# Optimization experiments

Hardware: AMD Instinct MI355X
Metric: run time of the kernel (lower is better)

The kernel has to match this reference:

```python
import jax, jax.numpy as jnp
import numpy as np

ALPHA = 0.2  # LeakyReLU negative slope
NEG_INF = -9e15


def setup_inputs() -> dict:
    key = jax.random.key(0)
    k1, k2, k3, k4 = jax.random.split(key, 4)
    N, F_in, F_out = 8192, 256, 64
    h = jax.random.normal(k1, (N, F_in), dtype=jnp.float32)
    adj = jax.random.randint(k2, (N, N), 0, 2, dtype=jnp.int32)
    # xavier-uniform-style scaling for params
    W = jax.random.normal(k3, (F_in, F_out), dtype=jnp.float32) * (1.0 / np.sqrt(F_in))
    a = jax.random.normal(k4, (2 * F_out, 1), dtype=jnp.float32) * (1.0 / np.sqrt(F_out))
    return {"h": h, "adj": adj, "W": W, "a": a}


def reference(h, adj, W, a):
    # Wh: [N, F_out]
    Wh = h @ W
    F_out = W.shape[1]
    a1 = a[:F_out, 0]   # attends to source (row i)
    a2 = a[F_out:, 0]   # attends to target (row j)
    f1 = Wh @ a1        # [N]
    f2 = Wh @ a2        # [N]
    # e[i, j] = leakyrelu(Wh_i . a1 + Wh_j . a2)  == original repeat/cat math
    e = jax.nn.leaky_relu(f1[:, None] + f2[None, :], negative_slope=ALPHA)
    attention = jnp.where(adj > 0, e, NEG_INF)
    attention = jax.nn.softmax(attention, axis=1)
    # dropout omitted (eval / deterministic reference)
    h_prime = attention @ Wh  # [N, F_out]
    return jax.nn.elu(h_prime)
```

## Files before the change

kernel.cpp:

```cpp
#include <hip/hip_runtime.h>
#include <hip/hip_bf16.h>
#include <stdint.h>

#define N 8192
#define FIN 256
#define FOUT 64
#define QSPLIT 8
#define NTASK (512 * QSPLIT)
#define JLEN (N / QSPLIT)
#define NITER (JLEN / 64)

typedef __attribute__((ext_vector_type(8))) short s8v;
typedef __attribute__((ext_vector_type(4))) float f4v;

__device__ __forceinline__ uint32_t f2bf(float f) {
  uint32_t u = __float_as_uint(f);
  return (u + 0x7FFFu + ((u >> 16) & 1u)) >> 16;
}

__global__ __launch_bounds__(256) void gat_prep(
    const float* __restrict__ h, const float* __restrict__ W,
    const float* __restrict__ a,
    float* __restrict__ f1, float* __restrict__ f2,
    uint16_t* __restrict__ whT)
{
  const int c = threadIdx.x & 63;
  const int wave = threadIdx.x >> 6;
  const int i0 = blockIdx.x * 16 + wave * 4;
  float acc[4] = {0.f, 0.f, 0.f, 0.f};
  #pragma unroll 8
  for (int k = 0; k < FIN; ++k) {
    float wv = W[k * FOUT + c];
    #pragma unroll
    for (int r = 0; r < 4; ++r)
      acc[r] += h[(size_t)(i0 + r) * FIN + k] * wv;
  }
  uint32_t b0 = f2bf(acc[0]), b1 = f2bf(acc[1]), b2 = f2bf(acc[2]), b3 = f2bf(acc[3]);
  int2 pk;
  pk.x = (int)(b0 | (b1 << 16));
  pk.y = (int)(b2 | (b3 << 16));
  *(int2*)(whT + (size_t)c * N + i0) = pk;

  const float a1 = a[c], a2 = a[FOUT + c];
  #pragma unroll
  for (int r = 0; r < 4; ++r) {
    float v1 = acc[r] * a1;
    float v2 = acc[r] * a2;
    #pragma unroll
    for (int m = 32; m > 0; m >>= 1) {
      v1 += __shfl_xor(v1, m, 64);
      v2 += __shfl_xor(v2, m, 64);
    }
    if (c == 0) { f1[i0 + r] = v1; f2[i0 + r] = v2; }
  }
}

__device__ __forceinline__ s8v make_afrag_r(float f1v, int4 c0, int4 c1,
                                            float4 g0, float4 g1, float& den) {
  float e0 = f1v + g0.x; e0 = fmaxf(e0, 0.2f * e0); float w0 = (c0.x > 0) ? __expf(e0) : 0.f;
  float e1 = f1v + g0.y; e1 = fmaxf(e1, 0.2f * e1); float w1 = (c0.y > 0) ? __expf(e1) : 0.f;
  float e2 = f1v + g0.z; e2 = fmaxf(e2, 0.2f * e2); float w2 = (c0.z > 0) ? __expf(e2) : 0.f;
  float e3 = f1v + g0.w; e3 = fmaxf(e3, 0.2f * e3); float w3 = (c0.w > 0) ? __expf(e3) : 0.f;
  float e4 = f1v + g1.x; e4 = fmaxf(e4, 0.2f * e4); float w4 = (c1.x > 0) ? __expf(e4) : 0.f;
  float e5 = f1v + g1.y; e5 = fmaxf(e5, 0.2f * e5); float w5 = (c1.y > 0) ? __expf(e5) : 0.f;
  float e6 = f1v + g1.z; e6 = fmaxf(e6, 0.2f * e6); float w6 = (c1.z > 0) ? __expf(e6) : 0.f;
  float e7 = f1v + g1.w; e7 = fmaxf(e7, 0.2f * e7); float w7 = (c1.w > 0) ? __expf(e7) : 0.f;
  uint32_t b0 = f2bf(w0), b1 = f2bf(w1), b2 = f2bf(w2), b3 = f2bf(w3);
  uint32_t b4 = f2bf(w4), b5 = f2bf(w5), b6 = f2bf(w6), b7 = f2bf(w7);
  den += __uint_as_float(b0 << 16) + __uint_as_float(b1 << 16)
       + __uint_as_float(b2 << 16) + __uint_as_float(b3 << 16)
       + __uint_as_float(b4 << 16) + __uint_as_float(b5 << 16)
       + __uint_as_float(b6 << 16) + __uint_as_float(b7 << 16);
  union { s8v v; uint32_t u[4]; } r;
  r.u[0] = b0 | (b1 << 16);
  r.u[1] = b2 | (b3 << 16);
  r.u[2] = b4 | (b5 << 16);
  r.u[3] = b6 | (b7 << 16);
  return r.v;
}

__global__ __launch_bounds__(256) void gat_main2(
    const int* __restrict__ adj, const float* __restrict__ f1,
    const float* __restrict__ f2, const uint16_t* __restrict__ whT,
    float* __restrict__ pnum, float* __restrict__ pden)
{
  const int t = threadIdx.x;
  const int wave = t >> 6;
  const int lane = t & 63;
  const int task = blockIdx.x * 4 + wave;
  const int group = task / QSPLIT;
  const int quarter = task % QSPLIT;
  const int i0 = group * 16;
  const int jb = quarter * JLEN;
  const int m  = lane & 15;
  const int kg = lane >> 4;

  const float f1v = f1[i0 + m];
  const int*      ap  = adj + (size_t)(i0 + m) * N + jb + kg * 8;
  const float*    fp  = f2 + jb + kg * 8;
  const uint16_t* bp0 = whT + (size_t)m * N + jb + kg * 8;

  f4v acc0 = {0.f, 0.f, 0.f, 0.f};
  f4v acc1 = acc0, acc2 = acc0, acc3 = acc0;
  float den = 0.f;

  int4   pc0 = *(const int4*)(ap);
  int4   pc1 = *(const int4*)(ap + 4);
  int4   pc2 = *(const int4*)(ap + 32);
  int4   pc3 = *(const int4*)(ap + 36);
  float4 pg0 = *(const float4*)(fp);
  float4 pg1 = *(const float4*)(fp + 4);
  float4 pg2 = *(const float4*)(fp + 32);
  float4 pg3 = *(const float4*)(fp + 36);

  #pragma unroll 1
  for (int jc = 0; jc < NITER; ++jc) {
    const int j0 = jc * 64;
    int4 c0 = pc0, c1 = pc1, c2 = pc2, c3 = pc3;
    float4 g0 = pg0, g1 = pg1, g2 = pg2, g3 = pg3;
    if (jc + 1 < NITER) {
      const int jn = j0 + 64;
      pc0 = *(const int4*)(ap + jn);
      pc1 = *(const int4*)(ap + jn + 4);
      pc2 = *(const int4*)(ap + jn + 32);
      pc3 = *(const int4*)(ap + jn + 36);
      pg0 = *(const float4*)(fp + jn);
      pg1 = *(const float4*)(fp + jn + 4);
      pg2 = *(const float4*)(fp + jn + 32);
      pg3 = *(const float4*)(fp + jn + 36);
    }
    s8v a0 = make_afrag_r(f1v, c0, c1, g0, g1, den);
    s8v a1 = make_afrag_r(f1v, c2, c3, g2, g3, den);
    const uint16_t* bp = bp0 + j0;
    s8v b00 = *(const s8v*)(bp);
    s8v b01 = *(const s8v*)(bp + 32);
    s8v b10 = *(const s8v*)(bp + 16 * N);
    s8v b11 = *(const s8v*)(bp + 16 * N + 32);
    s8v b20 = *(const s8v*)(bp + 32 * N);
    s8v b21 = *(const s8v*)(bp + 32 * N + 32);
    s8v b30 = *(const s8v*)(bp + 48 * N);
    s8v b31 = *(const s8v*)(bp + 48 * N + 32);
    acc0 = __builtin_amdgcn_mfma_f32_16x16x32_bf16(a0, b00, acc0, 0, 0, 0);
    acc0 = __builtin_amdgcn_mfma_f32_16x16x32_bf16(a1, b01, acc0, 0, 0, 0);
    acc1 = __builtin_amdgcn_mfma_f32_16x16x32_bf16(a0, b10, acc1, 0, 0, 0);
    acc1 = __builtin_amdgcn_mfma_f32_16x16x32_bf16(a1, b11, acc1, 0, 0, 0);
    acc2 = __builtin_amdgcn_mfma_f32_16x16x32_bf16(a0, b20, acc2, 0, 0, 0);
    acc2 = __builtin_amdgcn_mfma_f32_16x16x32_bf16(a1, b21, acc2, 0, 0, 0);
    acc3 = __builtin_amdgcn_mfma_f32_16x16x32_bf16(a0, b30, acc3, 0, 0, 0);
    acc3 = __builtin_amdgcn_mfma_f32_16x16x32_bf16(a1, b31, acc3, 0, 0, 0);
  }

  den += __shfl_xor(den, 16, 64);
  den += __shfl_xor(den, 32, 64);

  float* np = pnum + (size_t)task * (16 * 64);
  #pragma unroll
  for (int r = 0; r < 4; ++r) {
    int row = kg * 4 + r;
    np[row * 64 +      m] = acc0[r];
    np[row * 64 + 16 + m] = acc1[r];
    np[row * 64 + 32 + m] = acc2[r];
    np[row * 64 + 48 + m] = acc3[r];
  }
  if (lane < 16) pden[task * 16 + m] = den;
}

__global__ __launch_bounds__(256) void gat_combine(
    const float* __restrict__ pnum, const float* __restrict__ pden,
    float* __restrict__ out)
{
  const int idx = blockIdx.x * 256 + threadIdx.x;
  const int i = idx >> 6;
  const int c = idx & 63;
  const int g = i >> 4;
  const int r = i & 15;
  const size_t base = (size_t)g * QSPLIT * 1024 + (size_t)r * 64 + c;
  float num = 0.f;
  #pragma unroll
  for (int q = 0; q < QSPLIT; ++q) num += pnum[base + (size_t)q * 1024];
  const int db = g * (QSPLIT * 16) + r;
  float den = 0.f;
  #pragma unroll
  for (int q = 0; q < QSPLIT; ++q) den += pden[db + q * 16];
  float hp = num / den;
  out[idx] = (hp > 0.f) ? hp : (__expf(hp) - 1.f);
}

extern "C" void kernel_launch(void* const* d_in, const int* in_sizes, int n_in,
                              void* d_out, int out_size, void* d_ws, size_t ws_size,
                              hipStream_t stream) {
  const float* h   = (const float*)d_in[0];
  const int*   adj = (const int*)d_in[1];
  const float* W   = (const float*)d_in[2];
  const float* a   = (const float*)d_in[3];
  float* out = (float*)d_out;

  float* f1 = (float*)d_ws;
  float* f2 = f1 + N;
  uint16_t* whT = (uint16_t*)(f2 + N);
  float* pnum = (float*)(whT + (size_t)FOUT * N);
  float* pden = pnum + (size_t)NTASK * 16 * 64;

  gat_prep<<<N / 16, 256, 0, stream>>>(h, W, a, f1, f2, whT);
  gat_main2<<<NTASK / 4, 256, 0, stream>>>(adj, f1, f2, whT, pnum, pden);
  gat_combine<<<(N * FOUT) / 256, 256, 0, stream>>>(pnum, pden, out);
}
```

Baseline: 421.9 us.

## Fuse split-K combine into main kernel via LDS reduction and MFMA denominator

Each block now handles one 16-row group with 8 waves splitting the j range, and reduces the partial numerators and denominators through shared memory. This removes the global partial-sum buffers and the separate combine kernel launch. The softmax denominator is now computed by an extra MFMA against a vector of ones instead of scalar adds of the bf16-rounded weights. Scalar bf16 rounding is also swapped for the packed conversion intrinsic. The trade-off is larger 512-thread blocks, 36KB of LDS per block, and two extra MFMAs per iteration.

```diff
diff --git a/kernel.cpp b/kernel.cpp
--- a/kernel.cpp
+++ b/kernel.cpp
@@ -5,9 +5,8 @@
 #define N 8192
 #define FIN 256
 #define FOUT 64
-#define QSPLIT 8
-#define NTASK (512 * QSPLIT)
-#define JLEN (N / QSPLIT)
+#define WPB 8
+#define JLEN (N / WPB)
 #define NITER (JLEN / 64)
 
 typedef __attribute__((ext_vector_type(8))) short s8v;
@@ -16,6 +15,13 @@
 __device__ __forceinline__ uint32_t f2bf(float f) {
   uint32_t u = __float_as_uint(f);
   return (u + 0x7FFFu + ((u >> 16) & 1u)) >> 16;
+}
+
+__device__ __forceinline__ uint32_t pk2(float x, float y) {
+  __hip_bfloat162 p = __float22bfloat162_rn(make_float2(x, y));
+  union { __hip_bfloat162 b; uint32_t u; } c;
+  c.b = p;
+  return c.u;
 }
 
 __global__ __launch_bounds__(256) void gat_prep(
@@ -35,10 +41,9 @@
     for (int r = 0; r < 4; ++r)
       acc[r] += h[(size_t)(i0 + r) * FIN + k] * wv;
   }
-  uint32_t b0 = f2bf(acc[0]), b1 = f2bf(acc[1]), b2 = f2bf(acc[2]), b3 = f2bf(acc[3]);
   int2 pk;
-  pk.x = (int)(b0 | (b1 << 16));
-  pk.y = (int)(b2 | (b3 << 16));
+  pk.x = (int)pk2(acc[0], acc[1]);
+  pk.y = (int)pk2(acc[2], acc[3]);
   *(int2*)(whT + (size_t)c * N + i0) = pk;
 
   const float a1 = a[c], a2 = a[FOUT + c];
@@ -56,7 +61,7 @@
 }
 
 __device__ __forceinline__ s8v make_afrag_r(float f1v, int4 c0, int4 c1,
-                                            float4 g0, float4 g1, float& den) {
+                                            float4 g0, float4 g1) {
   float e0 = f1v + g0.x; e0 = fmaxf(e0, 0.2f * e0); float w0 = (c0.x > 0) ? __expf(e0) : 0.f;
   float e1 = f1v + g0.y; e1 = fmaxf(e1, 0.2f * e1); float w1 = (c0.y > 0) ? __expf(e1) : 0.f;
   float e2 = f1v + g0.z; e2 = fmaxf(e2, 0.2f * e2); float w2 = (c0.z > 0) ? __expf(e2) : 0.f;
@@ -65,33 +70,27 @@
   float e5 = f1v + g1.y; e5 = fmaxf(e5, 0.2f * e5); float w5 = (c1.y > 0) ? __expf(e5) : 0.f;
   float e6 = f1v + g1.z; e6 = fmaxf(e6, 0.2f * e6); float w6 = (c1.z > 0) ? __expf(e6) : 0.f;
   float e7 = f1v + g1.w; e7 = fmaxf(e7, 0.2f * e7); float w7 = (c1.w > 0) ? __expf(e7) : 0.f;
-  uint32_t b0 = f2bf(w0), b1 = f2bf(w1), b2 = f2bf(w2), b3 = f2bf(w3);
-  uint32_t b4 = f2bf(w4), b5 = f2bf(w5), b6 = f2bf(w6), b7 = f2bf(w7);
-  den += __uint_as_float(b0 << 16) + __uint_as_float(b1 << 16)
-       + __uint_as_float(b2 << 16) + __uint_as_float(b3 << 16)
-       + __uint_as_float(b4 << 16) + __uint_as_float(b5 << 16)
-       + __uint_as_float(b6 << 16) + __uint_as_float(b7 << 16);
   union { s8v v; uint32_t u[4]; } r;
-  r.u[0] = b0 | (b1 << 16);
-  r.u[1] = b2 | (b3 << 16);
-  r.u[2] = b4 | (b5 << 16);
-  r.u[3] = b6 | (b7 << 16);
+  r.u[0] = pk2(w0, w1);
+  r.u[1] = pk2(w2, w3);
+  r.u[2] = pk2(w4, w5);
+  r.u[3] = pk2(w6, w7);
   return r.v;
 }
 
-__global__ __launch_bounds__(256) void gat_main2(
+__global__ __launch_bounds__(512) void gat_fused(
     const int* __restrict__ adj, const float* __restrict__ f1,
     const float* __restrict__ f2, const uint16_t* __restrict__ whT,
-    float* __restrict__ pnum, float* __restrict__ pden)
+    float* __restrict__ out)
 {
+  __shared__ float red[WPB][16][64];
+  __shared__ float redd[WPB][16];
+
   const int t = threadIdx.x;
   const int wave = t >> 6;
   const int lane = t & 63;
-  const int task = blockIdx.x * 4 + wave;
-  const int group = task / QSPLIT;
-  const int quarter = task % QSPLIT;
-  const int i0 = group * 16;
-  const int jb = quarter * JLEN;
+  const int i0 = blockIdx.x * 16;
+  const int jb = wave * JLEN;
   const int m  = lane & 15;
   const int kg = lane >> 4;
 
@@ -101,8 +100,10 @@
   const uint16_t* bp0 = whT + (size_t)m * N + jb + kg * 8;
 
   f4v acc0 = {0.f, 0.f, 0.f, 0.f};
-  f4v acc1 = acc0, acc2 = acc0, acc3 = acc0;
-  float den = 0.f;
+  f4v acc1 = acc0, acc2 = acc0, acc3 = acc0, accd = acc0;
+  union { s8v v; uint32_t u[4]; } ones;
+  ones.u[0] = 0x3F803F80u; ones.u[1] = 0x3F803F80u;
+  ones.u[2] = 0x3F803F80u; ones.u[3] = 0x3F803F80u;
 
   int4   pc0 = *(const int4*)(ap);
   int4   pc1 = *(const int4*)(ap + 4);
@@ -129,8 +130,8 @@
       pg2 = *(const float4*)(fp + jn + 32);
       pg3 = *(const float4*)(fp + jn + 36);
     }
-    s8v a0 = make_afrag_r(f1v, c0, c1, g0, g1, den);
-    s8v a1 = make_afrag_r(f1v, c2, c3, g2, g3, den);
+    s8v a0 = make_afrag_r(f1v, c0, c1, g0, g1);
+    s8v a1 = make_afrag_r(f1v, c2, c3, g2, g3);
     const uint16_t* bp = bp0 + j0;
     s8v b00 = *(const s8v*)(bp);
     s8v b01 = *(const s8v*)(bp + 32);
@@ -148,42 +149,37 @@
     acc2 = __builtin_amdgcn_mfma_f32_16x16x32_bf16(a1, b21, acc2, 0, 0, 0);
     acc3 = __builtin_amdgcn_mfma_f32_16x16x32_bf16(a0, b30, acc3, 0, 0, 0);
     acc3 = __builtin_amdgcn_mfma_f32_16x16x32_bf16(a1, b31, acc3, 0, 0, 0);
-  }
-
-  den += __shfl_xor(den, 16, 64);
-  den += __shfl_xor(den, 32, 64);
-
-  float* np = pnum + (size_t)task * (16 * 64);
+    accd = __builtin_amdgcn_mfma_f32_16x16x32_bf16(a0, ones.v, accd, 0, 0, 0);
+    accd = __builtin_amdgcn_mfma_f32_16x16x32_bf16(a1, ones.v, accd, 0, 0, 0);
+  }
+
   #pragma unroll
   for (int r = 0; r < 4; ++r) {
     int row = kg * 4 + r;
-    np[row * 64 +      m] = acc0[r];
-    np[row * 64 + 16 + m] = acc1[r];
-    np[row * 64 + 32 + m] = acc2[r];
-    np[row * 64 + 48 + m] = acc3[r];
-  }
-  if (lane < 16) pden[task * 16 + m] = den;
-}
-
-__global__ __launch_bounds__(256) void gat_combine(
-    const float* __restrict__ pnum, const float* __restrict__ pden,
-    float* __restrict__ out)
-{
-  const int idx = blockIdx.x * 256 + threadIdx.x;
-  const int i = idx >> 6;
-  const int c = idx & 63;
-  const int g = i >> 4;
-  const int r = i & 15;
-  const size_t base = (size_t)g * QSPLIT * 1024 + (size_t)r * 64 + c;
-  float num = 0.f;
+    red[wave][row][     m] = acc0[r];
+    red[wave][row][16 + m] = acc1[r];
+    red[wave][row][32 + m] = acc2[r];
+    red[wave][row][48 + m] = acc3[r];
+  }
+  if (m == 0) {
+    #pragma unroll
+    for (int r = 0; r < 4; ++r) redd[wave][kg * 4 + r] = accd[r];
+  }
+  __syncthreads();
+
   #pragma unroll
-  for (int q = 0; q < QSPLIT; ++q) num += pnum[base + (size_t)q * 1024];
-  const int db = g * (QSPLIT * 16) + r;
-  float den = 0.f;
-  #pragma unroll
-  for (int q = 0; q < QSPLIT; ++q) den += pden[db + q * 16];
-  float hp = num / den;
-  out[idx] = (hp > 0.f) ? hp : (__expf(hp) - 1.f);
+  for (int idx = t; idx < 16 * 64; idx += 512) {
+    const int row = idx >> 6;
+    const int col = idx & 63;
+    float num = 0.f, den = 0.f;
+    #pragma unroll
+    for (int w = 0; w < WPB; ++w) {
+      num += red[w][row][col];
+      den += redd[w][row];
+    }
+    float hp = num / den;
+    out[(size_t)(i0 + row) * FOUT + col] = (hp > 0.f) ? hp : (__expf(hp) - 1.f);
+  }
 }
 
 extern "C" void kernel_launch(void* const* d_in, const int* in_sizes, int n_in,
@@ -198,10 +194,7 @@
   float* f1 = (float*)d_ws;
   float* f2 = f1 + N;
   uint16_t* whT = (uint16_t*)(f2 + N);
-  float* pnum = (float*)(whT + (size_t)FOUT * N);
-  float* pden = pnum + (size_t)NTASK * 16 * 64;
 
   gat_prep<<<N / 16, 256, 0, stream>>>(h, W, a, f1, f2, whT);
-  gat_main2<<<NTASK / 4, 256, 0, stream>>>(adj, f1, f2, whT, pnum, pden);
-  gat_combine<<<(N * FOUT) / 256, 256, 0, stream>>>(pnum, pden, out);
-}
+  gat_fused<<<N / 16, 512, 0, stream>>>(adj, f1, f2, whT, out);
+}
```

Measured after the change: 437.2 us. 1.04x slower.
